# Kernel tuning notes

Measured on AMD Instinct MI355X. Metric: run time of the kernel, lower is better.

Reference implementation:

```python
import jax, jax.numpy as jnp
import numpy as np

ROWS, COLS, NFEAT = 128, 128, 256
BATCH = 4096


def setup_inputs() -> dict:
    key = jax.random.key(0)
    k1, k2 = jax.random.split(key)
    xb = jax.random.normal(k1, (BATCH, NFEAT), dtype=jnp.float32)
    weights = jax.random.normal(k2, (ROWS, COLS, NFEAT), dtype=jnp.float32)
    return {"xb": xb, "weights": weights}


def reference(xb, weights):
    # Flatten codebook: (M, F) with M = rows*cols
    w = weights.reshape(-1, NFEAT)
    # Pairwise Euclidean distances via ||a||^2 + ||b||^2 - 2 a.b (single GEMM)
    a2 = jnp.sum(xb * xb, axis=-1, keepdims=True)            # (B, 1)
    b2 = jnp.sum(w * w, axis=-1)                             # (M,)
    d2 = a2 + b2[None, :] - 2.0 * jnp.einsum('bf,mf->bm', xb, w)  # (B, M)
    distances = jnp.sqrt(jnp.maximum(d2, 0.0))
    # BMU: argmin over codebook, converted to 2D map indices
    min_idxs = jnp.argmin(distances, axis=-1)                # (B,)
    bmus = jnp.stack([min_idxs // COLS, min_idxs % COLS], axis=-1)  # (B, 2)
    return bmus
```

## Files before the change

kernel.cpp:

```cpp
#include <hip/hip_runtime.h>
#include <cfloat>

#define NFEAT 256
#define BATCH 4096
#define MTOT  16384
#define NSTRIP 8
#define STRIPW 2048
#define NH 16
#define UMARGIN 0.75f

typedef __attribute__((ext_vector_type(8))) short bf16x8;
typedef __attribute__((ext_vector_type(4))) float f32x4;

#define GP(p)   ((const __attribute__((address_space(1))) void*)(p))
#define LDSP(p) ((__attribute__((address_space(3))) void*)(p))

__device__ __forceinline__ unsigned bf16pack(float a, float b) {
    unsigned ua = __float_as_uint(a), ub = __float_as_uint(b);
    unsigned ra = (ua + 0x7fffu + ((ua >> 16) & 1u)) >> 16;
    unsigned rb = (ub + 0x7fffu + ((ub >> 16) & 1u)) >> 16;
    return ra | (rb << 16);
}

__global__ __launch_bounds__(256) void prep_kernel(const float* __restrict__ xb,
                                                   const float* __restrict__ w,
                                                   uint2* __restrict__ Abf,
                                                   uint2* __restrict__ Bbf,
                                                   float* __restrict__ a2,
                                                   float* __restrict__ b2) {
    int gid  = blockIdx.x * blockDim.x + threadIdx.x;
    int row  = gid >> 6;
    int lane = gid & 63;
    const float* src;
    uint2* dst;
    float* nrm;
    if (row < MTOT) {
        src = w + (size_t)row * NFEAT;  dst = Bbf + (size_t)row * 64;  nrm = b2 + row;
    } else {
        int r = row - MTOT;
        src = xb + (size_t)r * NFEAT;   dst = Abf + (size_t)r * 64;    nrm = a2 + r;
    }
    float4 v = ((const float4*)src)[lane];
    dst[lane] = make_uint2(bf16pack(v.x, v.y), bf16pack(v.z, v.w));
    float s = v.x * v.x + v.y * v.y + v.z * v.z + v.w * v.w;
    #pragma unroll
    for (int off = 32; off > 0; off >>= 1) s += __shfl_down(s, off);
    if (lane == 0) *nrm = s;
}

__global__ __launch_bounds__(512, 2) void som_mfma_kernel(
        const unsigned short* __restrict__ Abf, const unsigned short* __restrict__ Bbf,
        const float* __restrict__ b2, float* __restrict__ part) {
    __shared__ char smem[139264];

    const int t = threadIdx.x, l = t & 63;
    const int wid = t >> 6;
    const int wm = wid >> 2;
    const int wc = wid & 3;
    const int strip = blockIdx.x & 7;
    const int m0 = (blockIdx.x >> 3) * 128;
    const int ns0 = strip * STRIPW;

    const char* gA = (const char*)Abf
                   + (size_t)(m0 + wm * 64 + (l & 15)) * 512 + (l >> 4) * 16;
    bf16x8 afr[4][8];
    #pragma unroll
    for (int m = 0; m < 4; ++m)
        #pragma unroll
        for (int kk = 0; kk < 8; ++kk)
            afr[m][kk] = *(const bf16x8*)(gA + (size_t)m * 16 * 512 + kk * 64);

    const int rowt = t >> 5;
    const int swzcol = ((t & 31) << 4) ^ ((rowt & 7) << 4);
    const char* gB = (const char*)Bbf + (size_t)(ns0 + rowt) * 512 + swzcol;

    __builtin_amdgcn_global_load_lds(GP((const char*)b2 + (size_t)ns0 * 4 + t * 16),
                                     LDSP(smem + 131072 + t * 16), 16, 0, 0);
    #pragma unroll
    for (int i = 0; i < 8; ++i)
        __builtin_amdgcn_global_load_lds(GP(gB + i * 8192),
                                         LDSP(smem + t * 16 + i * 8192), 16, 0, 0);
    #pragma unroll
    for (int i = 0; i < 8; ++i)
        __builtin_amdgcn_global_load_lds(GP(gB + 65536 + i * 8192),
                                         LDSP(smem + 65536 + t * 16 + i * 8192), 16, 0, 0);

    #pragma unroll
    for (int m = 0; m < 4; ++m)
        #pragma unroll
        for (int kk = 0; kk < 8; ++kk)
            asm volatile("" : "+v"(afr[m][kk]));

    float r0[4][4], r1[4][4];
    #pragma unroll
    for (int m = 0; m < 4; ++m)
        #pragma unroll
        for (int j = 0; j < 4; ++j) { r0[m][j] = -FLT_MAX; r1[m][j] = -FLT_MAX; }

    for (int h = 0; h < NH; ++h) {
        if (h < NH - 1) asm volatile("s_waitcnt vmcnt(8)" ::: "memory");
        else            asm volatile("s_waitcnt vmcnt(0)" ::: "memory");
        __builtin_amdgcn_s_barrier();
        asm volatile("" ::: "memory");

        const char* bufB = smem + ((h & 1) << 16);
        const int c0 = h * 128 + wc * 32 + (l & 15);
        const float b20 = -0.5f * *(const float*)(smem + 131072 + c0 * 4);
        const float b21 = -0.5f * *(const float*)(smem + 131072 + c0 * 4 + 64);

        f32x4 acc[4][2];
        #pragma unroll
        for (int m = 0; m < 4; ++m) {
            acc[m][0] = (f32x4){b20, b20, b20, b20};
            acc[m][1] = (f32x4){b21, b21, b21, b21};
        }

        #pragma unroll
        for (int kk = 0; kk < 8; ++kk) {
            const int swz = (kk * 64 + (l >> 4) * 16) ^ ((l & 7) << 4);
            bf16x8 bf0 = *(const bf16x8*)(bufB + (wc * 32 + (l & 15)) * 512 + swz);
            bf16x8 bf1 = *(const bf16x8*)(bufB + (wc * 32 + 16 + (l & 15)) * 512 + swz);
            #pragma unroll
            for (int m = 0; m < 4; ++m) {
                acc[m][0] = __builtin_amdgcn_mfma_f32_16x16x32_bf16(afr[m][kk], bf0, acc[m][0], 0, 0, 0);
                acc[m][1] = __builtin_amdgcn_mfma_f32_16x16x32_bf16(afr[m][kk], bf1, acc[m][1], 0, 0, 0);
            }
        }

        #pragma unroll
        for (int n = 0; n < 2; ++n) {
            const unsigned idn = (unsigned)(h * 2 + n);
            #pragma unroll
            for (int m = 0; m < 4; ++m)
                #pragma unroll
                for (int j = 0; j < 4; ++j) {
                    float p = __uint_as_float((__float_as_uint(acc[m][n][j]) & 0xFFFFFFE0u) | idn);
                    float nr1 = __builtin_amdgcn_fmed3f(r0[m][j], r1[m][j], p);
                    r0[m][j] = fmaxf(r0[m][j], p);
                    r1[m][j] = nr1;
                }
        }

        asm volatile("" ::: "memory");
        __builtin_amdgcn_s_barrier();
        asm volatile("" ::: "memory");
        if (h + 2 < NH) {
            const char* gBn = gB + (size_t)(h + 2) * 65536;
            char* dst = smem + ((h & 1) << 16) + t * 16;
            #pragma unroll
            for (int i = 0; i < 8; ++i)
                __builtin_amdgcn_global_load_lds(GP(gBn + i * 8192),
                                                 LDSP(dst + i * 8192), 16, 0, 0);
        }
    }

    float* sm = (float*)smem;
    #pragma unroll
    for (int m = 0; m < 4; ++m)
        #pragma unroll
        for (int j = 0; j < 4; ++j) {
            unsigned u0 = __float_as_uint(r0[m][j]);
            unsigned u1 = __float_as_uint(r1[m][j]);
            u0 = (u0 & 0xFFFFF800u) | ((u0 & 31u) << 6) | ((unsigned)wc << 4) | (unsigned)(l & 15);
            u1 = (u1 & 0xFFFFF800u) | ((u1 & 31u) << 6) | ((unsigned)wc << 4) | (unsigned)(l & 15);
            float v0 = __uint_as_float(u0), v1 = __uint_as_float(u1);
            #pragma unroll
            for (int off = 1; off < 16; off <<= 1) {
                float o0 = __shfl_xor(v0, off), o1 = __shfl_xor(v1, off);
                float nv1 = fmaxf(fminf(v0, o0), fmaxf(v1, o1));
                v0 = fmaxf(v0, o0);
                v1 = nv1;
            }
            if ((l & 15) == 0) {
                int row_l = wm * 64 + m * 16 + (l >> 4) * 4 + j;
                sm[row_l * 8 + wc * 2 + 0] = v0;
                sm[row_l * 8 + wc * 2 + 1] = v1;
            }
        }
    __syncthreads();
    if (t < 128) {
        float V0 = -FLT_MAX, V1 = -FLT_MAX;
        #pragma unroll
        for (int q = 0; q < 4; ++q) {
            float a0 = sm[t * 8 + q * 2], a1 = sm[t * 8 + q * 2 + 1];
            float nv1 = fmaxf(fminf(V0, a0), fmaxf(V1, a1));
            V0 = fmaxf(V0, a0);
            V1 = nv1;
        }
        ((float2*)part)[(size_t)(m0 + t) * NSTRIP + strip] = make_float2(V0, V1);
    }
}

__global__ __launch_bounds__(256) void refine_kernel(
        const float* __restrict__ xb, const float* __restrict__ w,
        const float* __restrict__ a2, const float* __restrict__ b2,
        const float* __restrict__ part, int* __restrict__ out) {
    const int t = threadIdx.x, l = t & 63;
    const int row = blockIdx.x * 4 + (t >> 6);

    const float* pr = part + (size_t)row * (NSTRIP * 2);
    float v = (l < NSTRIP * 2) ? pr[l] : -FLT_MAX;
    float mx = v;
    #pragma unroll
    for (int off = 1; off < 64; off <<= 1) mx = fmaxf(mx, __shfl_xor(mx, off));
    const float cut = mx - UMARGIN;

    unsigned long long key = ~0ull;
    if (l < NSTRIP * 2 && v >= cut) {
        unsigned b = __float_as_uint(v);
        int lane4 = b & 15, wcb = (b >> 4) & 3, inner = (b >> 6) & 31;
        int col = (l >> 1) * STRIPW + (inner >> 1) * 128 + wcb * 32
                + (inner & 1) * 16 + lane4;
        const float4* xr = (const float4*)(xb + (size_t)row * NFEAT);
        const float4* wr = (const float4*)(w + (size_t)col * NFEAT);
        float s0 = 0.f, s1 = 0.f, s2 = 0.f, s3 = 0.f;
        #pragma unroll
        for (int k = 0; k < 16; ++k) {
            float4 x0 = xr[4 * k + 0], w0 = wr[4 * k + 0];
            float4 x1 = xr[4 * k + 1], w1 = wr[4 * k + 1];
            float4 x2 = xr[4 * k + 2], w2 = wr[4 * k + 2];
            float4 x3 = xr[4 * k + 3], w3 = wr[4 * k + 3];
            s0 += x0.x * w0.x + x0.y * w0.y + x0.z * w0.z + x0.w * w0.w;
            s1 += x1.x * w1.x + x1.y * w1.y + x1.z * w1.z + x1.w * w1.w;
            s2 += x2.x * w2.x + x2.y * w2.y + x2.z * w2.z + x2.w * w2.w;
            s3 += x3.x * w3.x + x3.y * w3.y + x3.z * w3.z + x3.w * w3.w;
        }
        float dot = (s0 + s1) + (s2 + s3);
        float dd = a2[row] + b2[col] - 2.f * dot;
        float s = sqrtf(fmaxf(dd, 0.f));
        key = ((unsigned long long)__float_as_uint(s) << 32) | (unsigned)col;
    }
    #pragma unroll
    for (int off = 1; off < 64; off <<= 1) {
        unsigned long long o = __shfl_xor(key, off);
        key = o < key ? o : key;
    }
    if (l == 0) {
        int idx = (int)(key & 0xffffffffu);
        out[2 * row]     = idx >> 7;
        out[2 * row + 1] = idx & 127;
    }
}

extern "C" void kernel_launch(void* const* d_in, const int* in_sizes, int n_in,
                              void* d_out, int out_size, void* d_ws, size_t ws_size,
                              hipStream_t stream) {
    const float* xb = (const float*)d_in[0];
    const float* w  = (const float*)d_in[1];
    int* out = (int*)d_out;

    char* ws = (char*)d_ws;
    unsigned short* Abf = (unsigned short*)ws;
    unsigned short* Bbf = (unsigned short*)(ws + (2u << 20));
    float* a2   = (float*)(ws + (10u << 20));
    float* b2   = (float*)(ws + (10u << 20) + (64u << 10));
    float* part = (float*)(ws + (10u << 20) + (128u << 10));

    prep_kernel<<<((MTOT + BATCH) * 64) / 256, 256, 0, stream>>>(xb, w, (uint2*)Abf,
                                                                 (uint2*)Bbf, a2, b2);
    som_mfma_kernel<<<256, 512, 0, stream>>>(Abf, Bbf, b2, part);
    refine_kernel<<<BATCH / 4, 256, 0, stream>>>(xb, w, a2, b2, part, out);
}
```

Before: 75.77 us.

## Give each wave private LDS B-buffers to drop per-iteration block barriers

Each wave now streams its own 16-column slice of the codebook strip into a private LDS region, using global_load_lds in an MFMA-fragment-ready layout. This removes the two workgroup barriers per iteration and the swizzled shared reads. The strip is processed in 32 steps of 64 columns instead of 16 steps of 128, each wave doing 4 MFMAs per k-step instead of 8, and the refine kernel's column decoding is updated to match. The trade-off is less work per synchronization-free step and loss of B-tile sharing across the two wave rows, so the two waves that share a wc each load the same data.

```diff
diff --git a/kernel.cpp b/kernel.cpp
--- a/kernel.cpp
+++ b/kernel.cpp
@@ -6,7 +6,7 @@
 #define MTOT  16384
 #define NSTRIP 8
 #define STRIPW 2048
-#define NH 16
+#define NH 32
 #define UMARGIN 0.75f
 
 typedef __attribute__((ext_vector_type(8))) short bf16x8;
@@ -70,20 +70,20 @@
         for (int kk = 0; kk < 8; ++kk)
             afr[m][kk] = *(const bf16x8*)(gA + (size_t)m * 16 * 512 + kk * 64);
 
-    const int rowt = t >> 5;
-    const int swzcol = ((t & 31) << 4) ^ ((rowt & 7) << 4);
-    const char* gB = (const char*)Bbf + (size_t)(ns0 + rowt) * 512 + swzcol;
-
     __builtin_amdgcn_global_load_lds(GP((const char*)b2 + (size_t)ns0 * 4 + t * 16),
                                      LDSP(smem + 131072 + t * 16), 16, 0, 0);
+
+    char* const reg0 = smem + wid * 16384;
+    const char* gBw = (const char*)Bbf
+                    + (size_t)(ns0 + wc * 16 + (l & 15)) * 512 + (l >> 4) * 16;
     #pragma unroll
     for (int i = 0; i < 8; ++i)
-        __builtin_amdgcn_global_load_lds(GP(gB + i * 8192),
-                                         LDSP(smem + t * 16 + i * 8192), 16, 0, 0);
+        __builtin_amdgcn_global_load_lds(GP(gBw + i * 64),
+                                         LDSP(reg0 + i * 1024 + l * 16), 16, 0, 0);
     #pragma unroll
     for (int i = 0; i < 8; ++i)
-        __builtin_amdgcn_global_load_lds(GP(gB + 65536 + i * 8192),
-                                         LDSP(smem + 65536 + t * 16 + i * 8192), 16, 0, 0);
+        __builtin_amdgcn_global_load_lds(GP(gBw + 32768 + i * 64),
+                                         LDSP(reg0 + 8192 + i * 1024 + l * 16), 16, 0, 0);
 
     #pragma unroll
     for (int m = 0; m < 4; ++m)
@@ -91,69 +91,59 @@
         for (int kk = 0; kk < 8; ++kk)
             asm volatile("" : "+v"(afr[m][kk]));
 
+    asm volatile("s_waitcnt vmcnt(16)" ::: "memory");
+    __builtin_amdgcn_s_barrier();
+
     float r0[4][4], r1[4][4];
     #pragma unroll
     for (int m = 0; m < 4; ++m)
         #pragma unroll
         for (int j = 0; j < 4; ++j) { r0[m][j] = -FLT_MAX; r1[m][j] = -FLT_MAX; }
+
+    const char* gBn = gBw + 2 * 32768;
 
     for (int h = 0; h < NH; ++h) {
         if (h < NH - 1) asm volatile("s_waitcnt vmcnt(8)" ::: "memory");
         else            asm volatile("s_waitcnt vmcnt(0)" ::: "memory");
-        __builtin_amdgcn_s_barrier();
-        asm volatile("" ::: "memory");
-
-        const char* bufB = smem + ((h & 1) << 16);
-        const int c0 = h * 128 + wc * 32 + (l & 15);
-        const float b20 = -0.5f * *(const float*)(smem + 131072 + c0 * 4);
-        const float b21 = -0.5f * *(const float*)(smem + 131072 + c0 * 4 + 64);
-
-        f32x4 acc[4][2];
-        #pragma unroll
-        for (int m = 0; m < 4; ++m) {
-            acc[m][0] = (f32x4){b20, b20, b20, b20};
-            acc[m][1] = (f32x4){b21, b21, b21, b21};
-        }
+
+        const char* buf = reg0 + ((h & 1) << 13);
+        const float b2c = -0.5f * *(const float*)(smem + 131072
+                              + (h * 64 + wc * 16 + (l & 15)) * 4);
+        f32x4 acc[4];
+        #pragma unroll
+        for (int m = 0; m < 4; ++m) acc[m] = (f32x4){b2c, b2c, b2c, b2c};
 
         #pragma unroll
         for (int kk = 0; kk < 8; ++kk) {
-            const int swz = (kk * 64 + (l >> 4) * 16) ^ ((l & 7) << 4);
-            bf16x8 bf0 = *(const bf16x8*)(bufB + (wc * 32 + (l & 15)) * 512 + swz);
-            bf16x8 bf1 = *(const bf16x8*)(bufB + (wc * 32 + 16 + (l & 15)) * 512 + swz);
-            #pragma unroll
-            for (int m = 0; m < 4; ++m) {
-                acc[m][0] = __builtin_amdgcn_mfma_f32_16x16x32_bf16(afr[m][kk], bf0, acc[m][0], 0, 0, 0);
-                acc[m][1] = __builtin_amdgcn_mfma_f32_16x16x32_bf16(afr[m][kk], bf1, acc[m][1], 0, 0, 0);
+            bf16x8 bf = *(const bf16x8*)(buf + kk * 1024 + l * 16);
+            #pragma unroll
+            for (int m = 0; m < 4; ++m)
+                acc[m] = __builtin_amdgcn_mfma_f32_16x16x32_bf16(afr[m][kk], bf,
+                                                                 acc[m], 0, 0, 0);
+        }
+
+        const unsigned idn = (unsigned)h;
+        #pragma unroll
+        for (int m = 0; m < 4; ++m)
+            #pragma unroll
+            for (int j = 0; j < 4; ++j) {
+                float p = __uint_as_float((__float_as_uint(acc[m][j]) & 0xFFFFFFE0u) | idn);
+                float nr1 = __builtin_amdgcn_fmed3f(r0[m][j], r1[m][j], p);
+                r0[m][j] = fmaxf(r0[m][j], p);
+                r1[m][j] = nr1;
             }
-        }
-
-        #pragma unroll
-        for (int n = 0; n < 2; ++n) {
-            const unsigned idn = (unsigned)(h * 2 + n);
-            #pragma unroll
-            for (int m = 0; m < 4; ++m)
-                #pragma unroll
-                for (int j = 0; j < 4; ++j) {
-                    float p = __uint_as_float((__float_as_uint(acc[m][n][j]) & 0xFFFFFFE0u) | idn);
-                    float nr1 = __builtin_amdgcn_fmed3f(r0[m][j], r1[m][j], p);
-                    r0[m][j] = fmaxf(r0[m][j], p);
-                    r1[m][j] = nr1;
-                }
-        }
-
-        asm volatile("" ::: "memory");
-        __builtin_amdgcn_s_barrier();
-        asm volatile("" ::: "memory");
+
         if (h + 2 < NH) {
-            const char* gBn = gB + (size_t)(h + 2) * 65536;
-            char* dst = smem + ((h & 1) << 16) + t * 16;
+            char* dst = reg0 + ((h & 1) << 13);
             #pragma unroll
             for (int i = 0; i < 8; ++i)
-                __builtin_amdgcn_global_load_lds(GP(gBn + i * 8192),
-                                                 LDSP(dst + i * 8192), 16, 0, 0);
-        }
-    }
-
+                __builtin_amdgcn_global_load_lds(GP(gBn + i * 64),
+                                                 LDSP(dst + i * 1024 + l * 16), 16, 0, 0);
+        }
+        gBn += 32768;
+    }
+
+    __syncthreads();
     float* sm = (float*)smem;
     #pragma unroll
     for (int m = 0; m < 4; ++m)
@@ -208,9 +198,8 @@
     unsigned long long key = ~0ull;
     if (l < NSTRIP * 2 && v >= cut) {
         unsigned b = __float_as_uint(v);
-        int lane4 = b & 15, wcb = (b >> 4) & 3, inner = (b >> 6) & 31;
-        int col = (l >> 1) * STRIPW + (inner >> 1) * 128 + wcb * 32
-                + (inner & 1) * 16 + lane4;
+        int c = b & 15, wcb = (b >> 4) & 3, h = (b >> 6) & 31;
+        int col = (l >> 1) * STRIPW + h * 64 + wcb * 16 + c;
         const float4* xr = (const float4*)(xb + (size_t)row * NFEAT);
         const float4* wr = (const float4*)(w + (size_t)col * NFEAT);
         float s0 = 0.f, s1 = 0.f, s2 = 0.f, s3 = 0.f;
```

Measured after the change: 102.5 us. 1.35x slower.

## Split codebook into 16 narrower strips with 256-thread blocks and earlier prefetch

Applied to the files above, without the earlier changes.

The MFMA distance kernel now uses 512 blocks of 256 threads, each covering a 1024-column codebook strip with 64-column stages, instead of 256 blocks of 512 threads over 2048-column strips. LDS per block is halved, so more blocks can be resident, and the block-to-strip mapping is reordered. The next-stage global-to-LDS load is issued right after the MFMA loop rather than after the top-2 update, and MFMA issue priority is raised with s_setprio. Index packing in the top-2 keys and the refine decoding are adjusted to the new layout. The cost is twice as many partial candidates per row for the refine kernel to scan.

```diff
diff --git a/kernel.cpp b/kernel.cpp
--- a/kernel.cpp
+++ b/kernel.cpp
@@ -4,8 +4,8 @@
 #define NFEAT 256
 #define BATCH 4096
 #define MTOT  16384
-#define NSTRIP 8
-#define STRIPW 2048
+#define NSTRIP 16
+#define STRIPW 1024
 #define NH 16
 #define UMARGIN 0.75f
 
@@ -48,17 +48,18 @@
     if (lane == 0) *nrm = s;
 }
 
-__global__ __launch_bounds__(512, 2) void som_mfma_kernel(
+__global__ __launch_bounds__(256, 2) void som_mfma_kernel(
         const unsigned short* __restrict__ Abf, const unsigned short* __restrict__ Bbf,
         const float* __restrict__ b2, float* __restrict__ part) {
-    __shared__ char smem[139264];
+    __shared__ char smem[69632];
 
     const int t = threadIdx.x, l = t & 63;
     const int wid = t >> 6;
-    const int wm = wid >> 2;
-    const int wc = wid & 3;
-    const int strip = blockIdx.x & 7;
-    const int m0 = (blockIdx.x >> 3) * 128;
+    const int wm = wid >> 1;
+    const int wc = wid & 1;
+    const int x = blockIdx.x & 7, y = blockIdx.x >> 3;
+    const int strip = x * 2 + (y >> 5);
+    const int m0 = (y & 31) * 128;
     const int ns0 = strip * STRIPW;
 
     const char* gA = (const char*)Abf
@@ -69,33 +70,39 @@
         #pragma unroll
         for (int kk = 0; kk < 8; ++kk)
             afr[m][kk] = *(const bf16x8*)(gA + (size_t)m * 16 * 512 + kk * 64);
-
-    const int rowt = t >> 5;
-    const int swzcol = ((t & 31) << 4) ^ ((rowt & 7) << 4);
-    const char* gB = (const char*)Bbf + (size_t)(ns0 + rowt) * 512 + swzcol;
-
-    __builtin_amdgcn_global_load_lds(GP((const char*)b2 + (size_t)ns0 * 4 + t * 16),
-                                     LDSP(smem + 131072 + t * 16), 16, 0, 0);
-    #pragma unroll
-    for (int i = 0; i < 8; ++i)
-        __builtin_amdgcn_global_load_lds(GP(gB + i * 8192),
-                                         LDSP(smem + t * 16 + i * 8192), 16, 0, 0);
-    #pragma unroll
-    for (int i = 0; i < 8; ++i)
-        __builtin_amdgcn_global_load_lds(GP(gB + 65536 + i * 8192),
-                                         LDSP(smem + 65536 + t * 16 + i * 8192), 16, 0, 0);
-
     #pragma unroll
     for (int m = 0; m < 4; ++m)
         #pragma unroll
         for (int kk = 0; kk < 8; ++kk)
             asm volatile("" : "+v"(afr[m][kk]));
 
+    const int sbyte = ((t & 31) * 16) ^ ((t >> 5) << 4);
+    const char* gBs0 = (const char*)Bbf + (size_t)ns0 * 512
+                     + (size_t)(t >> 5) * 512 + sbyte;
+    const char* gBs1 = (const char*)Bbf + (size_t)ns0 * 512
+                     + (size_t)(t >> 5) * 512 + (sbyte ^ 128);
+#define STAGE(p, hh) {                                                           \
+        _Pragma("unroll")                                                        \
+        for (int i_ = 0; i_ < 8; ++i_) {                                         \
+            const char* s_ = ((i_ & 1) ? gBs1 : gBs0)                            \
+                           + (size_t)(hh) * 32768 + i_ * 4096;                   \
+            __builtin_amdgcn_global_load_lds(GP(s_),                             \
+                LDSP(smem + (p) * 32768 + i_ * 4096 + t * 16), 16, 0, 0);        \
+        } }
+
+    __builtin_amdgcn_global_load_lds(GP((const char*)b2 + (size_t)ns0 * 4 + t * 16),
+                                     LDSP(smem + 65536 + t * 16), 16, 0, 0);
+    STAGE(0, 0)
+    STAGE(1, 1)
+
     float r0[4][4], r1[4][4];
     #pragma unroll
     for (int m = 0; m < 4; ++m)
         #pragma unroll
         for (int j = 0; j < 4; ++j) { r0[m][j] = -FLT_MAX; r1[m][j] = -FLT_MAX; }
+
+    const int rswz = (l & 15) << 4;
+    const int cbyte0 = (wc * 32 + (l & 15)) * 512;
 
     for (int h = 0; h < NH; ++h) {
         if (h < NH - 1) asm volatile("s_waitcnt vmcnt(8)" ::: "memory");
@@ -103,10 +110,10 @@
         __builtin_amdgcn_s_barrier();
         asm volatile("" ::: "memory");
 
-        const char* bufB = smem + ((h & 1) << 16);
-        const int c0 = h * 128 + wc * 32 + (l & 15);
-        const float b20 = -0.5f * *(const float*)(smem + 131072 + c0 * 4);
-        const float b21 = -0.5f * *(const float*)(smem + 131072 + c0 * 4 + 64);
+        const char* buf = smem + ((h & 1) << 15);
+        const int c0 = h * 64 + wc * 32 + (l & 15);
+        const float b20 = -0.5f * *(const float*)(smem + 65536 + c0 * 4);
+        const float b21 = -0.5f * *(const float*)(smem + 65536 + c0 * 4 + 64);
 
         f32x4 acc[4][2];
         #pragma unroll
@@ -115,43 +122,38 @@
             acc[m][1] = (f32x4){b21, b21, b21, b21};
         }
 
+        __builtin_amdgcn_s_setprio(1);
         #pragma unroll
         for (int kk = 0; kk < 8; ++kk) {
-            const int swz = (kk * 64 + (l >> 4) * 16) ^ ((l & 7) << 4);
-            bf16x8 bf0 = *(const bf16x8*)(bufB + (wc * 32 + (l & 15)) * 512 + swz);
-            bf16x8 bf1 = *(const bf16x8*)(bufB + (wc * 32 + 16 + (l & 15)) * 512 + swz);
+            const int ko = (kk * 64 + (l >> 4) * 16) ^ rswz;
+            bf16x8 bf0 = *(const bf16x8*)(buf + cbyte0 + ko);
+            bf16x8 bf1 = *(const bf16x8*)(buf + cbyte0 + 8192 + ko);
             #pragma unroll
             for (int m = 0; m < 4; ++m) {
                 acc[m][0] = __builtin_amdgcn_mfma_f32_16x16x32_bf16(afr[m][kk], bf0, acc[m][0], 0, 0, 0);
                 acc[m][1] = __builtin_amdgcn_mfma_f32_16x16x32_bf16(afr[m][kk], bf1, acc[m][1], 0, 0, 0);
             }
         }
-
-        #pragma unroll
-        for (int n = 0; n < 2; ++n) {
-            const unsigned idn = (unsigned)(h * 2 + n);
+        __builtin_amdgcn_s_setprio(0);
+
+        asm volatile("" ::: "memory");
+        __builtin_amdgcn_s_barrier();
+        asm volatile("" ::: "memory");
+        if (h + 2 < NH) STAGE(h & 1, h + 2)
+
+        #pragma unroll
+        for (int nf = 0; nf < 2; ++nf) {
+            const unsigned idn = (unsigned)(h * 2 + nf);
             #pragma unroll
             for (int m = 0; m < 4; ++m)
                 #pragma unroll
                 for (int j = 0; j < 4; ++j) {
-                    float p = __uint_as_float((__float_as_uint(acc[m][n][j]) & 0xFFFFFFE0u) | idn);
+                    float p = __uint_as_float((__float_as_uint(acc[m][nf][j]) & 0xFFFFFFE0u) | idn);
                     float nr1 = __builtin_amdgcn_fmed3f(r0[m][j], r1[m][j], p);
                     r0[m][j] = fmaxf(r0[m][j], p);
                     r1[m][j] = nr1;
                 }
         }
-
-        asm volatile("" ::: "memory");
-        __builtin_amdgcn_s_barrier();
-        asm volatile("" ::: "memory");
-        if (h + 2 < NH) {
-            const char* gBn = gB + (size_t)(h + 2) * 65536;
-            char* dst = smem + ((h & 1) << 16) + t * 16;
-            #pragma unroll
-            for (int i = 0; i < 8; ++i)
-                __builtin_amdgcn_global_load_lds(GP(gBn + i * 8192),
-                                                 LDSP(dst + i * 8192), 16, 0, 0);
-        }
     }
 
     float* sm = (float*)smem;
@@ -161,8 +163,8 @@
         for (int j = 0; j < 4; ++j) {
             unsigned u0 = __float_as_uint(r0[m][j]);
             unsigned u1 = __float_as_uint(r1[m][j]);
-            u0 = (u0 & 0xFFFFF800u) | ((u0 & 31u) << 6) | ((unsigned)wc << 4) | (unsigned)(l & 15);
-            u1 = (u1 & 0xFFFFF800u) | ((u1 & 31u) << 6) | ((unsigned)wc << 4) | (unsigned)(l & 15);
+            u0 = (u0 & 0xFFFFFC00u) | ((u0 & 31u) << 5) | ((unsigned)wc << 4) | (unsigned)(l & 15);
+            u1 = (u1 & 0xFFFFFC00u) | ((u1 & 31u) << 5) | ((unsigned)wc << 4) | (unsigned)(l & 15);
             float v0 = __uint_as_float(u0), v1 = __uint_as_float(u1);
             #pragma unroll
             for (int off = 1; off < 16; off <<= 1) {
@@ -173,22 +175,19 @@
             }
             if ((l & 15) == 0) {
                 int row_l = wm * 64 + m * 16 + (l >> 4) * 4 + j;
-                sm[row_l * 8 + wc * 2 + 0] = v0;
-                sm[row_l * 8 + wc * 2 + 1] = v1;
+                sm[row_l * 4 + wc * 2 + 0] = v0;
+                sm[row_l * 4 + wc * 2 + 1] = v1;
             }
         }
     __syncthreads();
     if (t < 128) {
-        float V0 = -FLT_MAX, V1 = -FLT_MAX;
-        #pragma unroll
-        for (int q = 0; q < 4; ++q) {
-            float a0 = sm[t * 8 + q * 2], a1 = sm[t * 8 + q * 2 + 1];
-            float nv1 = fmaxf(fminf(V0, a0), fmaxf(V1, a1));
-            V0 = fmaxf(V0, a0);
-            V1 = nv1;
-        }
+        float a0 = sm[t * 4 + 0], a1 = sm[t * 4 + 1];
+        float c0 = sm[t * 4 + 2], c1 = sm[t * 4 + 3];
+        float V0 = fmaxf(a0, c0);
+        float V1 = fmaxf(fminf(a0, c0), fmaxf(a1, c1));
         ((float2*)part)[(size_t)(m0 + t) * NSTRIP + strip] = make_float2(V0, V1);
     }
+#undef STAGE
 }
 
 __global__ __launch_bounds__(256) void refine_kernel(
@@ -208,9 +207,9 @@
     unsigned long long key = ~0ull;
     if (l < NSTRIP * 2 && v >= cut) {
         unsigned b = __float_as_uint(v);
-        int lane4 = b & 15, wcb = (b >> 4) & 3, inner = (b >> 6) & 31;
-        int col = (l >> 1) * STRIPW + (inner >> 1) * 128 + wcb * 32
-                + (inner & 1) * 16 + lane4;
+        int lane4 = b & 15, wcb = (b >> 4) & 1, id5 = (b >> 5) & 31;
+        int col = (l >> 1) * STRIPW + (id5 >> 1) * 64 + wcb * 32
+                + (id5 & 1) * 16 + lane4;
         const float4* xr = (const float4*)(xb + (size_t)row * NFEAT);
         const float4* wr = (const float4*)(w + (size_t)col * NFEAT);
         float s0 = 0.f, s1 = 0.f, s2 = 0.f, s3 = 0.f;
@@ -258,6 +257,6 @@
 
     prep_kernel<<<((MTOT + BATCH) * 64) / 256, 256, 0, stream>>>(xb, w, (uint2*)Abf,
                                                                  (uint2*)Bbf, a2, b2);
-    som_mfma_kernel<<<256, 512, 0, stream>>>(Abf, Bbf, b2, part);
+    som_mfma_kernel<<<512, 256, 0, stream>>>(Abf, Bbf, b2, part);
     refine_kernel<<<BATCH / 4, 256, 0, stream>>>(xb, w, a2, b2, part, out);
 }
```

New measurement: 72.47 us. -4.4%, faster.
